# Kernel tuning notes

Hardware: AMD Instinct MI355X
Metric: run time of the kernel (lower is better)

The kernel has to match this reference:

```python
import jax, jax.numpy as jnp
import numpy as np

B, D = 16384, 2048          # batch, input_dim
N_TOP, N_CLASS = 8, 16      # top labels, bottom labels per top (uniform, contiguous ids)

def setup_inputs() -> dict:
    key = jax.random.key(0)
    k1, k2, k3, k4, k5 = jax.random.split(key, 5)
    INIT = 0.2  # matches init_weight uniform(-0.2, 0.2)
    return {
        "features": jax.random.normal(k1, (B, D), dtype=jnp.float32),
        "top_W": jax.random.uniform(k2, (N_TOP, D), minval=-INIT, maxval=INIT, dtype=jnp.float32),
        "top_b": jax.random.uniform(k3, (N_TOP,), minval=-INIT, maxval=INIT, dtype=jnp.float32),
        "bottom_W": jax.random.uniform(k4, (N_TOP, D, N_CLASS), minval=-INIT, maxval=INIT, dtype=jnp.float32),
        "bottom_b": jax.random.uniform(k5, (N_TOP, N_CLASS), minval=-INIT, maxval=INIT, dtype=jnp.float32),
    }

def reference(features, top_W, top_b, bottom_W, bottom_b):
    # dropout p=0.0 -> identity
    # top gate: linear + sigmoid, (b, n_top)
    top_scores = jax.nn.sigmoid(features @ top_W.T + top_b)
    # all per-top-label expert linears as one batched GEMM: (b, n_top, n_class)
    bottom_logits = jnp.einsum('bd,tdc->btc', features, bottom_W) + bottom_b
    bottom_scores = jax.nn.softmax(bottom_logits, axis=-1)
    # scatter-combine: bottom ids of top i are contiguous [i*N_CLASS, (i+1)*N_CLASS),
    # so the column scatter is a reshape. (b, n_bottom_labels)
    final_scores = (top_scores[:, :, None] * bottom_scores).reshape(features.shape[0], N_TOP * N_CLASS)
    return final_scores
```

## Files before the change

### kernel.cpp

```cpp
#include <hip/hip_runtime.h>


#define D_DIM 2048
#define NTILE 9
#define NCOLS 144

using f32x4 = float __attribute__((ext_vector_type(4)));
using half8 = _Float16 __attribute__((ext_vector_type(8)));

__global__ void prep_weights(const float* __restrict__ topW,
                             const float* __restrict__ botW,
                             _Float16* __restrict__ W) {
    int idx = blockIdx.x * blockDim.x + threadIdx.x;
    if (idx >= NCOLS * D_DIM) return;
    int n = idx >> 11;
    int k = idx & (D_DIM - 1);
    float v = 0.0f;
    if (n < 8) {
        v = topW[n * D_DIM + k];
    } else if (n < 136) {
        int t = (n - 8) >> 4, c = (n - 8) & 15;
        v = botW[(t * D_DIM + k) * 16 + c];
    }
    W[idx] = (_Float16)v;
}

__global__ __launch_bounds__(256, 4) void hc_fused(
        const float* __restrict__ feat, const _Float16* __restrict__ W,
        const float* __restrict__ top_b, const float* __restrict__ bot_b,
        float* __restrict__ out) {
    __shared__ float red[4][16][148];

    const int tid  = threadIdx.x;
    const int lane = tid & 63, wave = tid >> 6;
    const int quad = lane >> 4, low = lane & 15;
    const size_t row0 = (size_t)blockIdx.x * 16;

    const f32x4* Ap = (const f32x4*)(feat + (row0 + low) * D_DIM + wave * 512 + quad * 8);
    const _Float16* Bbase = W + (size_t)low * D_DIM + wave * 512 + quad * 8;

    f32x4 acc[NTILE];
    #pragma unroll
    for (int i = 0; i < NTILE; i++) acc[i] = (f32x4)0.0f;

    #pragma unroll 2
    for (int ks = 0; ks < 16; ks++) {
        f32x4 a0 = Ap[ks * 8];
        f32x4 a1 = Ap[ks * 8 + 1];
        half8 af;
        af[0] = (_Float16)a0[0]; af[1] = (_Float16)a0[1];
        af[2] = (_Float16)a0[2]; af[3] = (_Float16)a0[3];
        af[4] = (_Float16)a1[0]; af[5] = (_Float16)a1[1];
        af[6] = (_Float16)a1[2]; af[7] = (_Float16)a1[3];
        #pragma unroll
        for (int nt = 0; nt < NTILE; nt++) {
            half8 bf = *(const half8*)(Bbase + nt * 16 * D_DIM + ks * 32);
            acc[nt] = __builtin_amdgcn_mfma_f32_16x16x32_f16(af, bf, acc[nt], 0, 0, 0);
        }
    }

    #pragma unroll
    for (int nt = 0; nt < NTILE; nt++) {
        #pragma unroll
        for (int r = 0; r < 4; r++) {
            red[wave][quad * 4 + r][nt * 16 + low] = acc[nt][r];
        }
    }
    __syncthreads();

    const int row = tid >> 4;
    const int top = tid & 15;
    if (top < 8) {
        float zt = top_b[top];
        #pragma unroll
        for (int w = 0; w < 4; w++) zt += red[w][row][top];
        const float sig = 1.0f / (1.0f + __expf(-zt));

        float z[16];
        float zmax = -1e30f;
        #pragma unroll
        for (int c = 0; c < 16; c++) {
            float v = bot_b[top * 16 + c];
            #pragma unroll
            for (int w = 0; w < 4; w++) v += red[w][row][8 + top * 16 + c];
            z[c] = v;
            zmax = fmaxf(zmax, v);
        }
        float s = 0.0f;
        #pragma unroll
        for (int c = 0; c < 16; c++) { z[c] = __expf(z[c] - zmax); s += z[c]; }
        const float scale = sig / s;

        float* o = out + (row0 + row) * 128 + top * 16;
        #pragma unroll
        for (int c = 0; c < 16; c += 4) {
            f32x4 v = { z[c] * scale, z[c+1] * scale, z[c+2] * scale, z[c+3] * scale };
            *(f32x4*)(o + c) = v;
        }
    }
}

extern "C" void kernel_launch(void* const* d_in, const int* in_sizes, int n_in,
                              void* d_out, int out_size, void* d_ws, size_t ws_size,
                              hipStream_t stream) {
    const float* feat  = (const float*)d_in[0];
    const float* topW  = (const float*)d_in[1];
    const float* topB  = (const float*)d_in[2];
    const float* botW  = (const float*)d_in[3];
    const float* botB  = (const float*)d_in[4];
    float* out = (float*)d_out;
    _Float16* W = (_Float16*)d_ws;

    prep_weights<<<(NCOLS * D_DIM + 255) / 256, 256, 0, stream>>>(topW, botW, W);
    hc_fused<<<16384 / 16, 256, 0, stream>>>(feat, W, topB, botB, out);
}
```

Measured before the change: 250.4 us.

## Pre-swizzle fp16 weights into MFMA fragment order for coalesced loads

The weight prep kernel now writes the fp16 B matrix directly in per-lane MFMA fragment order, grouped by wave, k-step and n-tile. Each lane's 16-byte load then falls in a contiguous 1KB wavefront segment instead of being strided by the D row pitch. The main loop issues all nine B-fragment loads ahead of the MFMAs and is unrolled further, to hide load latency. This costs more registers and could lower occupancy. The prep kernel's source reads become more scattered.

```diff
diff --git a/kernel.cpp b/kernel.cpp
--- a/kernel.cpp
+++ b/kernel.cpp
@@ -10,23 +10,34 @@
 
 __global__ void prep_weights(const float* __restrict__ topW,
                              const float* __restrict__ botW,
-                             _Float16* __restrict__ W) {
+                             _Float16* __restrict__ S) {
     int idx = blockIdx.x * blockDim.x + threadIdx.x;
-    if (idx >= NCOLS * D_DIM) return;
-    int n = idx >> 11;
-    int k = idx & (D_DIM - 1);
-    float v = 0.0f;
-    if (n < 8) {
-        v = topW[n * D_DIM + k];
-    } else if (n < 136) {
-        int t = (n - 8) >> 4, c = (n - 8) & 15;
-        v = botW[(t * D_DIM + k) * 16 + c];
+    if (idx >= 4 * 16 * NTILE * 64) return;
+    int lane = idx & 63;
+    int tmp  = idx >> 6;
+    int nt   = tmp % NTILE;
+    int wks  = tmp / NTILE;
+    int n     = nt * 16 + (lane & 15);
+    int kbase = wks * 32 + (lane >> 4) * 8;
+
+    _Float16 v[8];
+    #pragma unroll
+    for (int j = 0; j < 8; j++) {
+        int k = kbase + j;
+        float x = 0.0f;
+        if (n < 8) {
+            x = topW[n * D_DIM + k];
+        } else if (n < 136) {
+            int t = (n - 8) >> 4, c = (n - 8) & 15;
+            x = botW[(t * D_DIM + k) * 16 + c];
+        }
+        v[j] = (_Float16)x;
     }
-    W[idx] = (_Float16)v;
+    *(half8*)(S + (size_t)idx * 8) = *(half8*)v;
 }
 
 __global__ __launch_bounds__(256, 4) void hc_fused(
-        const float* __restrict__ feat, const _Float16* __restrict__ W,
+        const float* __restrict__ feat, const _Float16* __restrict__ Bsw,
         const float* __restrict__ top_b, const float* __restrict__ bot_b,
         float* __restrict__ out) {
     __shared__ float red[4][16][148];
@@ -37,26 +48,28 @@
     const size_t row0 = (size_t)blockIdx.x * 16;
 
     const f32x4* Ap = (const f32x4*)(feat + (row0 + low) * D_DIM + wave * 512 + quad * 8);
-    const _Float16* Bbase = W + (size_t)low * D_DIM + wave * 512 + quad * 8;
+    const _Float16* Bw = Bsw + (size_t)wave * (16 * NTILE * 512) + lane * 8;
 
     f32x4 acc[NTILE];
     #pragma unroll
     for (int i = 0; i < NTILE; i++) acc[i] = (f32x4)0.0f;
 
-    #pragma unroll 2
+    #pragma unroll 4
     for (int ks = 0; ks < 16; ks++) {
         f32x4 a0 = Ap[ks * 8];
         f32x4 a1 = Ap[ks * 8 + 1];
+        half8 bf[NTILE];
+        #pragma unroll
+        for (int nt = 0; nt < NTILE; nt++)
+            bf[nt] = *(const half8*)(Bw + (ks * NTILE + nt) * 512);
         half8 af;
         af[0] = (_Float16)a0[0]; af[1] = (_Float16)a0[1];
         af[2] = (_Float16)a0[2]; af[3] = (_Float16)a0[3];
         af[4] = (_Float16)a1[0]; af[5] = (_Float16)a1[1];
         af[6] = (_Float16)a1[2]; af[7] = (_Float16)a1[3];
         #pragma unroll
-        for (int nt = 0; nt < NTILE; nt++) {
-            half8 bf = *(const half8*)(Bbase + nt * 16 * D_DIM + ks * 32);
-            acc[nt] = __builtin_amdgcn_mfma_f32_16x16x32_f16(af, bf, acc[nt], 0, 0, 0);
-        }
+        for (int nt = 0; nt < NTILE; nt++)
+            acc[nt] = __builtin_amdgcn_mfma_f32_16x16x32_f16(af, bf[nt], acc[nt], 0, 0, 0);
     }
 
     #pragma unroll
@@ -109,8 +122,8 @@
     const float* botW  = (const float*)d_in[3];
     const float* botB  = (const float*)d_in[4];
     float* out = (float*)d_out;
-    _Float16* W = (_Float16*)d_ws;
+    _Float16* Bsw = (_Float16*)d_ws;
 
-    prep_weights<<<(NCOLS * D_DIM + 255) / 256, 256, 0, stream>>>(topW, botW, W);
-    hc_fused<<<16384 / 16, 256, 0, stream>>>(feat, W, topB, botB, out);
+    prep_weights<<<(4 * 16 * NTILE * 64 + 255) / 256, 256, 0, stream>>>(topW, botW, Bsw);
+    hc_fused<<<16384 / 16, 256, 0, stream>>>(feat, Bsw, topB, botB, out);
 }
```

New measurement: 214.8 us. 1.17x faster.
